# Performance work log

Measured on AMD Instinct MI355X. Metric: run time of the kernel, lower is better.

## Reference

```python
import jax, jax.numpy as jnp
import numpy as np

B_, S, D = 4, 4096, 2048   # batch, seq, d_model
OUT = 2048
E, R = 8, 16               # num_experts, lora rank
ALPHA = 32.0
SCALING = ALPHA / R


def setup_inputs() -> dict:
    key = jax.random.key(0)
    ks = jax.random.split(key, 6)
    x = jax.random.normal(ks[0], (B_, S, D), dtype=jnp.float32)
    W_base = jax.random.normal(ks[1], (OUT, D), dtype=jnp.float32) * (D ** -0.5)
    b_base = jax.random.normal(ks[2], (OUT,), dtype=jnp.float32) * 0.01
    router_W = jax.random.normal(ks[3], (E, D), dtype=jnp.float32) * (D ** -0.5)
    A = jax.random.normal(ks[4], (E, R, D), dtype=jnp.float32) * (D ** -0.5)   # lora_A weights [E, r, in]
    Bw = jax.random.normal(ks[5], (E, OUT, R), dtype=jnp.float32) * 0.02       # lora_B weights [E, out, r]
    return {"x": x, "W_base": W_base, "b_base": b_base, "router_W": router_W, "A": A, "Bw": Bw}


def reference(x, W_base, b_base, router_W, A, Bw):
    # frozen base linear
    base_out = jnp.einsum('bsd,od->bso', x, W_base) + b_base
    # router on detached input, top-1 expert
    logits = jnp.einsum('bsd,ed->bse', jax.lax.stop_gradient(x), router_W)
    routing_probs = jax.nn.softmax(logits, axis=-1)
    expert_idx = jnp.argmax(routing_probs, axis=-1)                 # [B,S]
    onehot = jax.nn.one_hot(expert_idx, E, dtype=x.dtype)           # [B,S,E]
    # LoRA down-proj for all experts (cheap: r=16), mask to selected expert
    h = jnp.einsum('bsd,erd->bser', x, A)                           # [B,S,E,R]
    h = h * onehot[..., None]
    # up-proj, combine over experts (only selected one is nonzero)
    delta = jnp.einsum('bser,eor->bso', h, Bw)                      # [B,S,OUT]
    return base_out + delta * SCALING
```

## Files before the change

### kernel.cpp

```cpp
#include <hip/hip_runtime.h>

#define D_    2048
#define OUT_  2048
#define E_    8
#define R_    16
#define KX    2176
#define M_    16384
#define SCALING_F 2.0f

typedef unsigned short ushort_t;
typedef unsigned short ushort8 __attribute__((ext_vector_type(8)));
typedef __bf16 bf16x8 __attribute__((ext_vector_type(8)));
typedef float f32x4 __attribute__((ext_vector_type(4)));

__device__ __forceinline__ ushort_t f2bf(float f) {
  unsigned u = __float_as_uint(f);
  u += 0x7FFFu + ((u >> 16) & 1u);
  return (ushort_t)(u >> 16);
}

#define GLOAD16(gp, lp)                                                        \
  __builtin_amdgcn_global_load_lds(                                            \
      (const __attribute__((address_space(1))) void*)(gp),                     \
      (__attribute__((address_space(3))) void*)(lp), 16, 0, 0)

__global__ __launch_bounds__(256) void wprep_all_kernel(
    const float* __restrict__ W, const float* __restrict__ Bw,
    const float* __restrict__ A,
    ushort_t* __restrict__ wext, ushort_t* __restrict__ aext)
{
  const int bid = blockIdx.x;
  const int t = threadIdx.x;
  if (bid < OUT_) {
    const int o = bid;
    const float* wr = W + (size_t)o * D_ + t * 8;
    float4 v0 = *(const float4*)wr;
    float4 v1 = *(const float4*)(wr + 4);
    ushort8 wb;
    wb[0] = f2bf(v0.x); wb[1] = f2bf(v0.y); wb[2] = f2bf(v0.z); wb[3] = f2bf(v0.w);
    wb[4] = f2bf(v1.x); wb[5] = f2bf(v1.y); wb[6] = f2bf(v1.z); wb[7] = f2bf(v1.w);
    *(ushort8*)(wext + (size_t)o * KX + t * 8) = wb;
    if (t < E_ * R_) {
      const int e = t >> 4, r = t & 15;
      wext[(size_t)o * KX + D_ + t] = f2bf(Bw[((size_t)e * OUT_ + o) * R_ + r]);
    }
  } else {
    const size_t i = ((size_t)(bid - OUT_) * 256 + t) * 8;
    float4 v0 = *(const float4*)(A + i);
    float4 v1 = *(const float4*)(A + i + 4);
    ushort8 b;
    b[0] = f2bf(v0.x); b[1] = f2bf(v0.y); b[2] = f2bf(v0.z); b[3] = f2bf(v0.w);
    b[4] = f2bf(v1.x); b[5] = f2bf(v1.y); b[6] = f2bf(v1.z); b[7] = f2bf(v1.w);
    *(ushort8*)(aext + i) = b;
  }
}

#define HG_NKT (D_ / 64)

__global__ __launch_bounds__(256) void hrouter_kernel(
    const float* __restrict__ x,
    const float* __restrict__ rW,
    const ushort_t* __restrict__ Ae,
    ushort_t* __restrict__ xext)
{
  __shared__ __attribute__((aligned(16))) char lds[40960];
  __shared__ int esel[32];

  const int t = threadIdx.x;
  const int lane = t & 63, w = t >> 6;
  const int wr = w >> 1, wc = w & 1;
  const int lr = lane & 15, lg = lane >> 4;
  const int koff = (lr & 7) << 4;

  const int bm = blockIdx.x;
  const size_t row0 = (size_t)bm * 32;

  const int sg_row = t >> 3;
  const int sg_c = t & 7;
  const int sg_slotx = sg_c ^ (sg_row & 7);

  auto stageA = [&](int TT) {
    char* dst = lds + (TT & 1) * 20480 + 4096;
    #pragma unroll
    for (int g = 0; g < 4; ++g) {
      const int r = g * 32 + sg_row;
      GLOAD16(Ae + (size_t)r * D_ + TT * 64 + sg_slotx * 8,
              dst + g * 4096 + t * 16);
    }
  };
  auto putX = [&](int TT, const float4& a, const float4& b) {
    ushort8 xb;
    xb[0] = f2bf(a.x); xb[1] = f2bf(a.y); xb[2] = f2bf(a.z); xb[3] = f2bf(a.w);
    xb[4] = f2bf(b.x); xb[5] = f2bf(b.y); xb[6] = f2bf(b.z); xb[7] = f2bf(b.w);
    char* Xb = lds + (TT & 1) * 20480;
    *(ushort8*)(Xb + sg_row * 128 + sg_slotx * 16) = xb;
    *(ushort8*)(xext + (row0 + sg_row) * KX + TT * 64 + sg_c * 8) = xb;
  };

  float la[E_];
  #pragma unroll
  for (int e = 0; e < E_; ++e) la[e] = 0.f;
  auto accLogit = [&](int TT, const float4& a, const float4& b) {
    const float* wp = rW + TT * 64 + sg_c * 8;
    #pragma unroll
    for (int e = 0; e < E_; ++e) {
      float4 w0 = *(const float4*)(wp + (size_t)e * D_);
      float4 w1 = *(const float4*)(wp + (size_t)e * D_ + 4);
      la[e] += a.x * w0.x + a.y * w0.y + a.z * w0.z + a.w * w0.w
             + b.x * w1.x + b.y * w1.y + b.z * w1.z + b.w * w1.w;
    }
  };

  f32x4 acc[4] = {};

  {
    const float* xp = x + (row0 + sg_row) * D_ + sg_c * 8;
    float4 a = *(const float4*)xp;
    float4 b = *(const float4*)(xp + 4);
    stageA(0);
    putX(0, a, b);
    accLogit(0, a, b);
  }
  __syncthreads();

  for (int T = 0; T < HG_NKT; ++T) {
    float4 na, nb;
    const bool more = (T + 1 < HG_NKT);
    if (more) {
      const float* xp = x + (row0 + sg_row) * D_ + (T + 1) * 64 + sg_c * 8;
      na = *(const float4*)xp;
      nb = *(const float4*)(xp + 4);
      stageA(T + 1);
    }
    char* Xb = lds + (T & 1) * 20480;
    char* Ab = Xb + 4096;
    bf16x8 af[2], bfr[4][2];
    #pragma unroll
    for (int kk = 0; kk < 2; ++kk)
      af[kk] = *(const bf16x8*)(Xb + (wr * 16 + lr) * 128 + ((kk * 64 + lg * 16) ^ koff));
    #pragma unroll
    for (int nj = 0; nj < 4; ++nj) {
      const int R = wc * 64 + nj * 16 + lr;
      #pragma unroll
      for (int kk = 0; kk < 2; ++kk)
        bfr[nj][kk] = *(const bf16x8*)(Ab + R * 128 + ((kk * 64 + lg * 16) ^ koff));
    }
    #pragma unroll
    for (int nj = 0; nj < 4; ++nj)
      #pragma unroll
      for (int kk = 0; kk < 2; ++kk)
        acc[nj] = __builtin_amdgcn_mfma_f32_16x16x32_bf16(af[kk], bfr[nj][kk], acc[nj], 0, 0, 0);
    if (more) {
      putX(T + 1, na, nb);
      accLogit(T + 1, na, nb);
    }
    __syncthreads();
  }

  {
    double s[E_];
    #pragma unroll
    for (int e = 0; e < E_; ++e) s[e] = (double)la[e];
    #pragma unroll
    for (int off = 1; off <= 4; off <<= 1)
      #pragma unroll
      for (int e = 0; e < E_; ++e) s[e] += __shfl_xor(s[e], off, 64);
    int bi = 0; double best = s[0];
    #pragma unroll
    for (int e = 1; e < E_; ++e)
      if (s[e] > best) { best = s[e]; bi = e; }
    if (sg_c == 0) esel[sg_row] = bi;
  }
  __syncthreads();

  int er[4];
  #pragma unroll
  for (int rr = 0; rr < 4; ++rr)
    er[rr] = esel[wr * 16 + lg * 4 + rr];
  #pragma unroll
  for (int nj = 0; nj < 4; ++nj) {
    const int col = wc * 64 + nj * 16 + lr;
    const int ecol = wc * 4 + nj;
    #pragma unroll
    for (int rr = 0; rr < 4; ++rr) {
      const size_t row = row0 + wr * 16 + lg * 4 + rr;
      ushort_t v = (er[rr] == ecol) ? f2bf(acc[nj][rr] * SCALING_F) : (ushort_t)0;
      xext[row * KX + D_ + col] = v;
    }
  }
}

#define NKT (KX / 64)
#define NITER (NKT / 2)
#define NSTG (NKT * 4)

__global__ __launch_bounds__(512, 2) void gemm_kernel(
    const ushort_t* __restrict__ Ag,
    const ushort_t* __restrict__ Bg,
    const float* __restrict__ bias,
    float* __restrict__ C)
{
  __shared__ __attribute__((aligned(16))) char lds[131072];

  const int t = threadIdx.x;
  const int lane = t & 63, w = t >> 6;
  const int wm = w >> 2, wn = w & 3;
  const int lr = lane & 15, lg = lane >> 4;
  const int koff = (lr & 7) << 4;

  const int swz = (blockIdx.x & 7) * 64 + (blockIdx.x >> 3);
  const int bm = swz >> 3, bn = swz & 7;

  const int sg_row = t >> 3;
  const int sg_slotx = (t & 7) ^ ((t >> 3) & 7);
  const size_t aRow0 = (size_t)bm * 256;
  const size_t bRow0 = (size_t)bn * 256;

  auto stage = [&](int s) {
    if (s >= NSTG) return;
    const int TT = s >> 2, j = s & 3;
    const int isB = j >> 1, half = j & 1;
    const ushort_t* src = isB ? Bg : Ag;
    const size_t gr0 = (isB ? bRow0 : aRow0) + half * 128;
    char* dst = lds + (TT & 1) * 65536 + isB * 32768 + half * 16384;
    #pragma unroll
    for (int g = 0; g < 2; ++g) {
      const int r = g * 64 + sg_row;
      GLOAD16(src + (gr0 + r) * KX + TT * 64 + sg_slotx * 8,
              dst + g * 8192 + t * 16);
    }
  };

  f32x4 acc[8][4] = {};
  bf16x8 bq[4][2];

  stage(0); stage(1); stage(2); stage(3);
  stage(6); stage(7);
  asm volatile("s_waitcnt vmcnt(4)" ::: "memory");
  __builtin_amdgcn_s_barrier();

  for (int ii = 0; ii < NITER; ++ii) {
    #pragma unroll
    for (int p = 0; p < 8; ++p) {
      const int q = p & 3;
      char* Ab = lds + ((2 * ii + (p >> 2)) & 1) * 65536;
      char* Bb = Ab + 32768;
      bf16x8 aq[2][2];
      if (q == 0) {
        #pragma unroll
        for (int nj = 0; nj < 4; ++nj) {
          const int R = wn * 64 + nj * 16 + lr;
          #pragma unroll
          for (int kk = 0; kk < 2; ++kk)
            bq[nj][kk] = *(const bf16x8*)(Bb + R * 128 + ((kk * 64 + lg * 16) ^ koff));
        }
      }
      #pragma unroll
      for (int i = 0; i < 2; ++i) {
        const int R = wm * 128 + (q * 2 + i) * 16 + lr;
        #pragma unroll
        for (int kk = 0; kk < 2; ++kk)
          aq[i][kk] = *(const bf16x8*)(Ab + R * 128 + ((kk * 64 + lg * 16) ^ koff));
      }
      switch (p) {
        case 0: stage(4 * (2 * ii + 1) + 0); break;
        case 1: stage(4 * (2 * ii + 1) + 1); break;
        case 2: stage(4 * (2 * ii + 2) + 2); break;
        case 3: stage(4 * (2 * ii + 2) + 3); break;
        case 4: stage(4 * (2 * ii + 2) + 0); break;
        case 5: stage(4 * (2 * ii + 2) + 1); break;
        case 6: stage(4 * (2 * ii + 3) + 2); break;
        case 7: stage(4 * (2 * ii + 3) + 3); break;
      }
      if (q == 0) asm volatile("s_waitcnt lgkmcnt(8)" ::: "memory");
      __builtin_amdgcn_s_barrier();
      asm volatile("s_waitcnt lgkmcnt(0)" ::: "memory");
      __builtin_amdgcn_s_setprio(1);
      #pragma unroll
      for (int i = 0; i < 2; ++i)
        #pragma unroll
        for (int nj = 0; nj < 4; ++nj)
          #pragma unroll
          for (int kk = 0; kk < 2; ++kk)
            acc[q * 2 + i][nj] = __builtin_amdgcn_mfma_f32_16x16x32_bf16(
                aq[i][kk], bq[nj][kk], acc[q * 2 + i][nj], 0, 0, 0);
      __builtin_amdgcn_s_setprio(0);
      if (p == 3 || p == 7) {
        if (ii == NITER - 1) asm volatile("s_waitcnt vmcnt(0)" ::: "memory");
        else                 asm volatile("s_waitcnt vmcnt(4)" ::: "memory");
      }
      __builtin_amdgcn_s_barrier();
    }
  }

  #pragma unroll
  for (int nj = 0; nj < 4; ++nj) {
    const int col = bn * 256 + wn * 64 + nj * 16 + lr;
    const float bv = bias[col];
    #pragma unroll
    for (int mi = 0; mi < 8; ++mi) {
      const int row0 = bm * 256 + wm * 128 + mi * 16 + lg * 4;
      #pragma unroll
      for (int rr = 0; rr < 4; ++rr)
        C[(size_t)(row0 + rr) * OUT_ + col] = acc[mi][nj][rr] + bv;
    }
  }
}

extern "C" void kernel_launch(void* const* d_in, const int* in_sizes, int n_in,
                              void* d_out, int out_size, void* d_ws, size_t ws_size,
                              hipStream_t stream) {
  const float* x  = (const float*)d_in[0];
  const float* Wb = (const float*)d_in[1];
  const float* bb = (const float*)d_in[2];
  const float* rW = (const float*)d_in[3];
  const float* A  = (const float*)d_in[4];
  const float* Bw = (const float*)d_in[5];
  float* out = (float*)d_out;

  ushort_t* xext = (ushort_t*)d_ws;
  ushort_t* wext = (ushort_t*)((char*)d_ws + (size_t)M_ * KX * 2);
  ushort_t* aext = (ushort_t*)((char*)d_ws + (size_t)M_ * KX * 2
                                           + (size_t)OUT_ * KX * 2);

  wprep_all_kernel<<<OUT_ + (E_ * R_ * D_) / (256 * 8), 256, 0, stream>>>(Wb, Bw, A, wext, aext);
  hrouter_kernel<<<M_ / 32, 256, 0, stream>>>(x, rW, aext, xext);
  gemm_kernel<<<(M_ / 256) * (OUT_ / 256), 512, 0, stream>>>(xext, wext, bb, out);
}
```

Measured before the change: 238.1 us.

## Load router/LoRA-down operands directly into MFMA fragments, dropping LDS staging

Rewrites the router + LoRA down-projection kernel so each lane reads x and A straight from global memory into MFMA register fragments, without double-buffered LDS staging or per-tile barriers. Router logits are split across the two column waves (4 experts each) and combined through a small shared-memory reduction. This removes LDS traffic and many __syncthreads, but gives up coalesced staging. x is now read by two waves and A is re-read from global/L2 by every block without software prefetch, so the kernel may become latency-bound.

```diff
diff --git a/kernel.cpp b/kernel.cpp
--- a/kernel.cpp
+++ b/kernel.cpp
@@ -57,119 +57,86 @@
 
 #define HG_NKT (D_ / 64)
 
-__global__ __launch_bounds__(256) void hrouter_kernel(
+__global__ __launch_bounds__(256) void hrouter2_kernel(
     const float* __restrict__ x,
     const float* __restrict__ rW,
     const ushort_t* __restrict__ Ae,
     ushort_t* __restrict__ xext)
 {
-  __shared__ __attribute__((aligned(16))) char lds[40960];
+  __shared__ double lsum[2][2][16][4];
   __shared__ int esel[32];
 
   const int t = threadIdx.x;
   const int lane = t & 63, w = t >> 6;
   const int wr = w >> 1, wc = w & 1;
   const int lr = lane & 15, lg = lane >> 4;
-  const int koff = (lr & 7) << 4;
 
   const int bm = blockIdx.x;
   const size_t row0 = (size_t)bm * 32;
-
-  const int sg_row = t >> 3;
-  const int sg_c = t & 7;
-  const int sg_slotx = sg_c ^ (sg_row & 7);
-
-  auto stageA = [&](int TT) {
-    char* dst = lds + (TT & 1) * 20480 + 4096;
-    #pragma unroll
-    for (int g = 0; g < 4; ++g) {
-      const int r = g * 32 + sg_row;
-      GLOAD16(Ae + (size_t)r * D_ + TT * 64 + sg_slotx * 8,
-              dst + g * 4096 + t * 16);
-    }
-  };
-  auto putX = [&](int TT, const float4& a, const float4& b) {
-    ushort8 xb;
-    xb[0] = f2bf(a.x); xb[1] = f2bf(a.y); xb[2] = f2bf(a.z); xb[3] = f2bf(a.w);
-    xb[4] = f2bf(b.x); xb[5] = f2bf(b.y); xb[6] = f2bf(b.z); xb[7] = f2bf(b.w);
-    char* Xb = lds + (TT & 1) * 20480;
-    *(ushort8*)(Xb + sg_row * 128 + sg_slotx * 16) = xb;
-    *(ushort8*)(xext + (row0 + sg_row) * KX + TT * 64 + sg_c * 8) = xb;
-  };
-
-  float la[E_];
-  #pragma unroll
-  for (int e = 0; e < E_; ++e) la[e] = 0.f;
-  auto accLogit = [&](int TT, const float4& a, const float4& b) {
-    const float* wp = rW + TT * 64 + sg_c * 8;
-    #pragma unroll
-    for (int e = 0; e < E_; ++e) {
-      float4 w0 = *(const float4*)(wp + (size_t)e * D_);
-      float4 w1 = *(const float4*)(wp + (size_t)e * D_ + 4);
-      la[e] += a.x * w0.x + a.y * w0.y + a.z * w0.z + a.w * w0.w
-             + b.x * w1.x + b.y * w1.y + b.z * w1.z + b.w * w1.w;
-    }
-  };
-
+  const size_t arow = row0 + wr * 16 + lr;
+
+  float la[4] = {0.f, 0.f, 0.f, 0.f};
   f32x4 acc[4] = {};
 
+  const float* xrow = x + arow * D_;
+  ushort_t* xsrow = xext + arow * KX;
+
+  for (int T = 0; T < HG_NKT; ++T) {
+    const int c0 = T * 64 + lg * 8;
+    bf16x8 af[2];
+    #pragma unroll
+    for (int kk = 0; kk < 2; ++kk) {
+      const float* xp = xrow + c0 + kk * 32;
+      float4 a = *(const float4*)xp;
+      float4 b = *(const float4*)(xp + 4);
+      union { ushort8 u; bf16x8 h; } cv;
+      cv.u[0] = f2bf(a.x); cv.u[1] = f2bf(a.y); cv.u[2] = f2bf(a.z); cv.u[3] = f2bf(a.w);
+      cv.u[4] = f2bf(b.x); cv.u[5] = f2bf(b.y); cv.u[6] = f2bf(b.z); cv.u[7] = f2bf(b.w);
+      af[kk] = cv.h;
+      if (wc == 0)
+        *(ushort8*)(xsrow + c0 + kk * 32) = cv.u;
+      #pragma unroll
+      for (int j = 0; j < 4; ++j) {
+        const float* wp = rW + (size_t)(wc * 4 + j) * D_ + c0 + kk * 32;
+        float4 w0 = *(const float4*)wp;
+        float4 w1 = *(const float4*)(wp + 4);
+        la[j] += a.x * w0.x + a.y * w0.y + a.z * w0.z + a.w * w0.w
+               + b.x * w1.x + b.y * w1.y + b.z * w1.z + b.w * w1.w;
+      }
+    }
+    #pragma unroll
+    for (int nj = 0; nj < 4; ++nj) {
+      const size_t Rc = wc * 64 + nj * 16 + lr;
+      #pragma unroll
+      for (int kk = 0; kk < 2; ++kk) {
+        bf16x8 bfr = *(const bf16x8*)(Ae + Rc * D_ + c0 + kk * 32);
+        acc[nj] = __builtin_amdgcn_mfma_f32_16x16x32_bf16(af[kk], bfr, acc[nj], 0, 0, 0);
+      }
+    }
+  }
+
   {
-    const float* xp = x + (row0 + sg_row) * D_ + sg_c * 8;
-    float4 a = *(const float4*)xp;
-    float4 b = *(const float4*)(xp + 4);
-    stageA(0);
-    putX(0, a, b);
-    accLogit(0, a, b);
+    double s[4];
+    #pragma unroll
+    for (int j = 0; j < 4; ++j) s[j] = (double)la[j];
+    #pragma unroll
+    for (int off = 16; off <= 32; off <<= 1)
+      #pragma unroll
+      for (int j = 0; j < 4; ++j) s[j] += __shfl_xor(s[j], off, 64);
+    if (lg == 0) {
+      #pragma unroll
+      for (int j = 0; j < 4; ++j) lsum[wr][wc][lr][j] = s[j];
+    }
   }
   __syncthreads();
-
-  for (int T = 0; T < HG_NKT; ++T) {
-    float4 na, nb;
-    const bool more = (T + 1 < HG_NKT);
-    if (more) {
-      const float* xp = x + (row0 + sg_row) * D_ + (T + 1) * 64 + sg_c * 8;
-      na = *(const float4*)xp;
-      nb = *(const float4*)(xp + 4);
-      stageA(T + 1);
-    }
-    char* Xb = lds + (T & 1) * 20480;
-    char* Ab = Xb + 4096;
-    bf16x8 af[2], bfr[4][2];
-    #pragma unroll
-    for (int kk = 0; kk < 2; ++kk)
-      af[kk] = *(const bf16x8*)(Xb + (wr * 16 + lr) * 128 + ((kk * 64 + lg * 16) ^ koff));
-    #pragma unroll
-    for (int nj = 0; nj < 4; ++nj) {
-      const int R = wc * 64 + nj * 16 + lr;
-      #pragma unroll
-      for (int kk = 0; kk < 2; ++kk)
-        bfr[nj][kk] = *(const bf16x8*)(Ab + R * 128 + ((kk * 64 + lg * 16) ^ koff));
-    }
-    #pragma unroll
-    for (int nj = 0; nj < 4; ++nj)
-      #pragma unroll
-      for (int kk = 0; kk < 2; ++kk)
-        acc[nj] = __builtin_amdgcn_mfma_f32_16x16x32_bf16(af[kk], bfr[nj][kk], acc[nj], 0, 0, 0);
-    if (more) {
-      putX(T + 1, na, nb);
-      accLogit(T + 1, na, nb);
-    }
-    __syncthreads();
-  }
-
-  {
-    double s[E_];
-    #pragma unroll
-    for (int e = 0; e < E_; ++e) s[e] = (double)la[e];
-    #pragma unroll
-    for (int off = 1; off <= 4; off <<= 1)
-      #pragma unroll
-      for (int e = 0; e < E_; ++e) s[e] += __shfl_xor(s[e], off, 64);
-    int bi = 0; double best = s[0];
-    #pragma unroll
-    for (int e = 1; e < E_; ++e)
-      if (s[e] > best) { best = s[e]; bi = e; }
-    if (sg_c == 0) esel[sg_row] = bi;
+  if (wc == 0 && lg == 0) {
+    double best = lsum[wr][0][lr][0]; int bi = 0;
+    #pragma unroll
+    for (int e = 1; e < E_; ++e) {
+      double v = (e < 4) ? lsum[wr][0][lr][e] : lsum[wr][1][lr][e - 4];
+      if (v > best) { best = v; bi = e; }
+    }
+    esel[wr * 16 + lr] = bi;
   }
   __syncthreads();
 
@@ -324,6 +291,6 @@
                                            + (size_t)OUT_ * KX * 2);
 
   wprep_all_kernel<<<OUT_ + (E_ * R_ * D_) / (256 * 8), 256, 0, stream>>>(Wb, Bw, A, wext, aext);
-  hrouter_kernel<<<M_ / 32, 256, 0, stream>>>(x, rW, aext, xext);
+  hrouter2_kernel<<<M_ / 32, 256, 0, stream>>>(x, rW, aext, xext);
   gemm_kernel<<<(M_ / 256) * (OUT_ / 256), 512, 0, stream>>>(xext, wext, bb, out);
 }
```

Measured after the change: 330.6 us. 38.9% more time.

## Halve router block rows to 16 and rebalance waves over expert columns

Applied to the files above, without the earlier changes.

The fused router/LoRA-down kernel now processes 16 rows per block instead of 32, doubling the grid, with each wave computing 32 expert-rank columns for all 16 rows. Each thread now handles 4 x values per k-tile, and the logit reduction goes through a cross-wave LDS step. The intent is more blocks and occupancy to better hide the x-streaming latency. In exchange, the A-weight tile is reloaded twice as often and there is an extra barrier for the logit reduction.

```diff
diff --git a/kernel.cpp b/kernel.cpp
--- a/kernel.cpp
+++ b/kernel.cpp
@@ -56,105 +56,89 @@
 }
 
 #define HG_NKT (D_ / 64)
-
-__global__ __launch_bounds__(256) void hrouter_kernel(
+#define HR_BUF 18432
+
+__global__ __launch_bounds__(256) void hrouter3_kernel(
     const float* __restrict__ x,
     const float* __restrict__ rW,
     const ushort_t* __restrict__ Ae,
     ushort_t* __restrict__ xext)
 {
-  __shared__ __attribute__((aligned(16))) char lds[40960];
-  __shared__ int esel[32];
+  __shared__ __attribute__((aligned(16))) char lds[2 * HR_BUF];
+  __shared__ double lsum[16][E_];
+  __shared__ int esel[16];
 
   const int t = threadIdx.x;
   const int lane = t & 63, w = t >> 6;
-  const int wr = w >> 1, wc = w & 1;
   const int lr = lane & 15, lg = lane >> 4;
-  const int koff = (lr & 7) << 4;
 
   const int bm = blockIdx.x;
-  const size_t row0 = (size_t)bm * 32;
-
-  const int sg_row = t >> 3;
-  const int sg_c = t & 7;
-  const int sg_slotx = sg_c ^ (sg_row & 7);
+  const size_t row0 = (size_t)bm * 16;
+
+  const int srow = t >> 4;
+  const int sc   = t & 15;
 
   auto stageA = [&](int TT) {
-    char* dst = lds + (TT & 1) * 20480 + 4096;
+    char* dst = lds + (TT & 1) * HR_BUF + 2048;
     #pragma unroll
     for (int g = 0; g < 4; ++g) {
-      const int r = g * 32 + sg_row;
-      GLOAD16(Ae + (size_t)r * D_ + TT * 64 + sg_slotx * 8,
-              dst + g * 4096 + t * 16);
+      const int c = g * 256 + t;
+      const int row = c >> 3, slotx = (c & 7) ^ (row & 7);
+      GLOAD16(Ae + (size_t)row * D_ + TT * 64 + slotx * 8, dst + c * 16);
     }
   };
-  auto putX = [&](int TT, const float4& a, const float4& b) {
-    ushort8 xb;
-    xb[0] = f2bf(a.x); xb[1] = f2bf(a.y); xb[2] = f2bf(a.z); xb[3] = f2bf(a.w);
-    xb[4] = f2bf(b.x); xb[5] = f2bf(b.y); xb[6] = f2bf(b.z); xb[7] = f2bf(b.w);
-    char* Xb = lds + (TT & 1) * 20480;
-    *(ushort8*)(Xb + sg_row * 128 + sg_slotx * 16) = xb;
-    *(ushort8*)(xext + (row0 + sg_row) * KX + TT * 64 + sg_c * 8) = xb;
+  auto putX = [&](int TT, const float4& a) {
+    ushort4 xb;
+    xb.x = f2bf(a.x); xb.y = f2bf(a.y); xb.z = f2bf(a.z); xb.w = f2bf(a.w);
+    char* Xb = lds + (TT & 1) * HR_BUF;
+    const int cb = (((sc >> 1) ^ (srow & 7)) << 4) + (sc & 1) * 8;
+    *(ushort4*)(Xb + srow * 128 + cb) = xb;
+    *(ushort4*)(xext + (row0 + srow) * KX + TT * 64 + sc * 4) = xb;
   };
 
-  float la[E_];
-  #pragma unroll
-  for (int e = 0; e < E_; ++e) la[e] = 0.f;
-  auto accLogit = [&](int TT, const float4& a, const float4& b) {
-    const float* wp = rW + TT * 64 + sg_c * 8;
-    #pragma unroll
-    for (int e = 0; e < E_; ++e) {
-      float4 w0 = *(const float4*)(wp + (size_t)e * D_);
-      float4 w1 = *(const float4*)(wp + (size_t)e * D_ + 4);
-      la[e] += a.x * w0.x + a.y * w0.y + a.z * w0.z + a.w * w0.w
-             + b.x * w1.x + b.y * w1.y + b.z * w1.z + b.w * w1.w;
-    }
-  };
-
-  f32x4 acc[4] = {};
-
-  {
-    const float* xp = x + (row0 + sg_row) * D_ + sg_c * 8;
-    float4 a = *(const float4*)xp;
-    float4 b = *(const float4*)(xp + 4);
-    stageA(0);
-    putX(0, a, b);
-    accLogit(0, a, b);
-  }
+  float la[E_] = {};
+  f32x4 acc[2] = {};
+
+  const float* xrow = x + (row0 + srow) * D_;
+
+  float4 cur = *(const float4*)(xrow + sc * 4);
+  stageA(0);
+  putX(0, cur);
   __syncthreads();
 
   for (int T = 0; T < HG_NKT; ++T) {
-    float4 na, nb;
+    float4 nxt;
     const bool more = (T + 1 < HG_NKT);
     if (more) {
-      const float* xp = x + (row0 + sg_row) * D_ + (T + 1) * 64 + sg_c * 8;
-      na = *(const float4*)xp;
-      nb = *(const float4*)(xp + 4);
+      nxt = *(const float4*)(xrow + (T + 1) * 64 + sc * 4);
       stageA(T + 1);
     }
-    char* Xb = lds + (T & 1) * 20480;
-    char* Ab = Xb + 4096;
-    bf16x8 af[2], bfr[4][2];
+    #pragma unroll
+    for (int e = 0; e < E_; ++e) {
+      const float4 wv = *(const float4*)(rW + (size_t)e * D_ + T * 64 + sc * 4);
+      la[e] += cur.x * wv.x + cur.y * wv.y + cur.z * wv.z + cur.w * wv.w;
+    }
+    char* Xb = lds + (T & 1) * HR_BUF;
+    char* Ab = Xb + 2048;
+    bf16x8 af[2], bfr[2][2];
     #pragma unroll
     for (int kk = 0; kk < 2; ++kk)
-      af[kk] = *(const bf16x8*)(Xb + (wr * 16 + lr) * 128 + ((kk * 64 + lg * 16) ^ koff));
-    #pragma unroll
-    for (int nj = 0; nj < 4; ++nj) {
-      const int R = wc * 64 + nj * 16 + lr;
+      af[kk] = *(const bf16x8*)(Xb + lr * 128 + ((kk * 64 + lg * 16) ^ ((lr & 7) << 4)));
+    #pragma unroll
+    for (int nj = 0; nj < 2; ++nj) {
+      const int Rc = w * 32 + nj * 16 + lr;
       #pragma unroll
       for (int kk = 0; kk < 2; ++kk)
-        bfr[nj][kk] = *(const bf16x8*)(Ab + R * 128 + ((kk * 64 + lg * 16) ^ koff));
-    }
-    #pragma unroll
-    for (int nj = 0; nj < 4; ++nj)
+        bfr[nj][kk] = *(const bf16x8*)(Ab + Rc * 128 + ((kk * 64 + lg * 16) ^ ((Rc & 7) << 4)));
+    }
+    #pragma unroll
+    for (int nj = 0; nj < 2; ++nj)
       #pragma unroll
       for (int kk = 0; kk < 2; ++kk)
         acc[nj] = __builtin_amdgcn_mfma_f32_16x16x32_bf16(af[kk], bfr[nj][kk], acc[nj], 0, 0, 0);
-    if (more) {
-      putX(T + 1, na, nb);
-      accLogit(T + 1, na, nb);
-    }
+    if (more) putX(T + 1, nxt);
     __syncthreads();
+    cur = nxt;
   }
 
   {
@@ -162,28 +146,35 @@
     #pragma unroll
     for (int e = 0; e < E_; ++e) s[e] = (double)la[e];
     #pragma unroll
-    for (int off = 1; off <= 4; off <<= 1)
+    for (int off = 1; off <= 8; off <<= 1)
       #pragma unroll
       for (int e = 0; e < E_; ++e) s[e] += __shfl_xor(s[e], off, 64);
-    int bi = 0; double best = s[0];
+    if ((lane & 15) == 0) {
+      #pragma unroll
+      for (int e = 0; e < E_; ++e) lsum[w * 4 + (lane >> 4)][e] = s[e];
+    }
+  }
+  __syncthreads();
+  if (t < 16) {
+    double best = lsum[t][0]; int bi = 0;
     #pragma unroll
     for (int e = 1; e < E_; ++e)
-      if (s[e] > best) { best = s[e]; bi = e; }
-    if (sg_c == 0) esel[sg_row] = bi;
+      if (lsum[t][e] > best) { best = lsum[t][e]; bi = e; }
+    esel[t] = bi;
   }
   __syncthreads();
 
   int er[4];
   #pragma unroll
   for (int rr = 0; rr < 4; ++rr)
-    er[rr] = esel[wr * 16 + lg * 4 + rr];
+    er[rr] = esel[lg * 4 + rr];
   #pragma unroll
-  for (int nj = 0; nj < 4; ++nj) {
-    const int col = wc * 64 + nj * 16 + lr;
-    const int ecol = wc * 4 + nj;
+  for (int nj = 0; nj < 2; ++nj) {
+    const int col = w * 32 + nj * 16 + lr;
+    const int ecol = w * 2 + nj;
     #pragma unroll
     for (int rr = 0; rr < 4; ++rr) {
-      const size_t row = row0 + wr * 16 + lg * 4 + rr;
+      const size_t row = row0 + lg * 4 + rr;
       ushort_t v = (er[rr] == ecol) ? f2bf(acc[nj][rr] * SCALING_F) : (ushort_t)0;
       xext[row * KX + D_ + col] = v;
     }
@@ -324,6 +315,6 @@
                                            + (size_t)OUT_ * KX * 2);
 
   wprep_all_kernel<<<OUT_ + (E_ * R_ * D_) / (256 * 8), 256, 0, stream>>>(Wb, Bw, A, wext, aext);
-  hrouter_kernel<<<M_ / 32, 256, 0, stream>>>(x, rW, aext, xext);
+  hrouter3_kernel<<<M_ / 16, 256, 0, stream>>>(x, rW, aext, xext);
   gemm_kernel<<<(M_ / 256) * (OUT_ / 256), 512, 0, stream>>>(xext, wext, bb, out);
 }
```

Measured after the change: 246.8 us. 3.6% more time.
